# Kernel tuning notes

Measured on AMD Instinct MI355X. Metric: run time of the kernel, lower is better.

## Reference

```python
import jax, jax.numpy as jnp
import numpy as np

STRIDE = 4
IMG_H, IMG_W = 800, 1216
NMS_THRESH = 0.7
PRE_NMS = 1000
POST_NMS = 1000
MIN_SIZE = 0.0
SCALE_CLAMP = float(np.log(1000.0 / 16.0))  # detectron2 Box2BoxTransform clamp
A = 3  # anchors per location


def _cell_anchors():
    size = 32.0
    ars = jnp.array([0.5, 1.0, 2.0], jnp.float32)
    area = size * size
    w = jnp.sqrt(area / ars)
    h = ars * w
    return jnp.stack([-w / 2, -h / 2, w / 2, h / 2], axis=1)  # [A,4]


def _anchors(H, W):
    sx = jnp.arange(W, dtype=jnp.float32) * STRIDE
    sy = jnp.arange(H, dtype=jnp.float32) * STRIDE
    gy, gx = jnp.meshgrid(sy, sx, indexing='ij')
    shifts = jnp.stack([gx, gy, gx, gy], axis=-1).reshape(-1, 1, 4)  # [H*W,1,4]
    return (shifts + _cell_anchors()[None]).reshape(-1, 4)  # [H*W*A,4]


def _conv(x, w, b, pad):
    y = jax.lax.conv_general_dilated(x, w, (1, 1), pad,
                                     dimension_numbers=('NCHW', 'OIHW', 'NCHW'))
    return y + b[None, :, None, None]


def _decode(anchors, deltas):
    # anchors [M,4], deltas [N,M,4]; weights (1,1,1,1)
    wa = anchors[:, 2] - anchors[:, 0]
    ha = anchors[:, 3] - anchors[:, 1]
    cx = anchors[:, 0] + 0.5 * wa
    cy = anchors[:, 1] + 0.5 * ha
    dx, dy = deltas[..., 0], deltas[..., 1]
    dw = jnp.minimum(deltas[..., 2], SCALE_CLAMP)
    dh = jnp.minimum(deltas[..., 3], SCALE_CLAMP)
    px = dx * wa + cx
    py = dy * ha + cy
    pw = jnp.exp(dw) * wa
    ph = jnp.exp(dh) * ha
    return jnp.stack([px - 0.5 * pw, py - 0.5 * ph,
                      px + 0.5 * pw, py + 0.5 * ph], axis=-1)


def _iou_matrix(boxes):  # [K,4] -> [K,K]
    area = (boxes[:, 2] - boxes[:, 0]) * (boxes[:, 3] - boxes[:, 1])
    lt = jnp.maximum(boxes[:, None, :2], boxes[None, :, :2])
    rb = jnp.minimum(boxes[:, None, 2:], boxes[None, :, 2:])
    wh = jnp.clip(rb - lt, 0.0)
    inter = wh[..., 0] * wh[..., 1]
    return inter / jnp.maximum(area[:, None] + area[None, :] - inter, 1e-9)


def _nms_keep(boxes):
    # boxes already sorted by descending score; greedy NMS
    iou = _iou_matrix(boxes)
    K = boxes.shape[0]

    def step(sup, i):
        keep = ~sup[i]
        sup = sup | (keep & (iou[i] > NMS_THRESH))
        return sup, keep

    _, keep = jax.lax.scan(step, jnp.zeros(K, bool), jnp.arange(K))
    return keep


def setup_inputs() -> dict:
    key = jax.random.key(0)
    ks = jax.random.split(key, 4)
    features = jax.random.normal(ks[0], (2, 256, 200, 304), jnp.float32)
    w_conv = jax.random.normal(ks[1], (256, 256, 3, 3), jnp.float32) * 0.01
    b_conv = jnp.zeros((256,), jnp.float32)
    w_obj = jax.random.normal(ks[2], (3, 256, 1, 1), jnp.float32) * 0.01
    b_obj = jnp.zeros((3,), jnp.float32)
    w_delta = jax.random.normal(ks[3], (12, 256, 1, 1), jnp.float32) * 0.01
    b_delta = jnp.zeros((12,), jnp.float32)
    return {"features": features, "w_conv": w_conv, "b_conv": b_conv,
            "w_obj": w_obj, "b_obj": b_obj, "w_delta": w_delta, "b_delta": b_delta}


def reference(features, w_conv, b_conv, w_obj, b_obj, w_delta, b_delta):
    N, C, H, W = features.shape
    t = jax.nn.relu(_conv(features, w_conv, b_conv, 'SAME'))
    logits = _conv(t, w_obj, b_obj, 'VALID')            # [N,A,H,W]
    deltas = _conv(t, w_delta, b_delta, 'VALID')        # [N,4A,H,W]
    logits = logits.transpose(0, 2, 3, 1).reshape(N, -1)               # [N,H*W*A]
    deltas = deltas.reshape(N, A, 4, H, W).transpose(0, 3, 4, 1, 2).reshape(N, -1, 4)

    anchors = _anchors(H, W)                             # [H*W*A,4]
    boxes = _decode(anchors, deltas)                     # [N,M,4]
    boxes = jnp.stack([jnp.clip(boxes[..., 0], 0.0, IMG_W),
                       jnp.clip(boxes[..., 1], 0.0, IMG_H),
                       jnp.clip(boxes[..., 2], 0.0, IMG_W),
                       jnp.clip(boxes[..., 3], 0.0, IMG_H)], axis=-1)

    valid = ((boxes[..., 2] - boxes[..., 0]) >= MIN_SIZE) & \
            ((boxes[..., 3] - boxes[..., 1]) >= MIN_SIZE)
    scores = jnp.where(valid, logits, -jnp.inf)

    top_s, top_i = jax.lax.top_k(scores, PRE_NMS)                      # sorted desc
    top_b = jnp.take_along_axis(boxes, top_i[..., None], axis=1)       # [N,K,4]

    keep = jax.vmap(_nms_keep)(top_b)                                  # [N,K]
    s = jnp.where(keep, top_s, -jnp.inf)
    fin_s, fin_i = jax.lax.top_k(s, POST_NMS)                          # sorted desc (=final sort)
    fin_b = jnp.take_along_axis(top_b, fin_i[..., None], axis=1)
    fin_b = jnp.where(jnp.isfinite(fin_s)[..., None], fin_b, 0.0)
    return fin_b, fin_s
```

## Files before the change

kernel.cpp:

```cpp
#include <hip/hip_runtime.h>
#include <math.h>
#include <stdint.h>

#define CC 256
#define HH 200
#define WW 304
#define NN 2
#define HW 60800
#define MM 182400
#define KK 1000
#define HP 202
#define WP 306
#define SCALE_CLAMP_F 4.135166556742356f
#define NEG_SENTINEL -1.0e30f
#define CAND_CAP 2048

typedef __attribute__((ext_vector_type(8))) short short8;
typedef __attribute__((ext_vector_type(4))) float f32x4;

__device__ __forceinline__ unsigned short f2bf(float f) {
  unsigned u = __float_as_uint(f);
  u += 0x7FFFu + ((u >> 16) & 1u);
  return (unsigned short)(u >> 16);
}
__device__ __forceinline__ unsigned int fkey(float s) {
  unsigned int u = __float_as_uint(s);
  return (u & 0x80000000u) ? ~u : (u | 0x80000000u);
}
__device__ __forceinline__ float iou_ref(float4 a, float4 b) {
#pragma clang fp contract(off)
  float areaA = (a.z - a.x) * (a.w - a.y);
  float areaB = (b.z - b.x) * (b.w - b.y);
  float ltx = fmaxf(a.x, b.x), lty = fmaxf(a.y, b.y);
  float rbx = fminf(a.z, b.z), rby = fminf(a.w, b.w);
  float w = fmaxf(rbx - ltx, 0.0f), h = fmaxf(rby - lty, 0.0f);
  float inter = w * h;
  float denom = fmaxf(areaA + areaB - inter, 1e-9f);
  return inter / denom;
}
__device__ __forceinline__ void gload16(const void* g, void* l) {
  __builtin_amdgcn_global_load_lds(
      (const __attribute__((address_space(1))) unsigned int*)g,
      (__attribute__((address_space(3))) unsigned int*)l, 16, 0, 0);
}
__device__ __forceinline__ int swz(int byte) {
  return byte ^ (((byte >> 7) & 7) << 4);
}

__global__ __launch_bounds__(256) void pack_kernel(
    const float* __restrict__ w, unsigned short* __restrict__ wt_b,
    const float* __restrict__ in, unsigned short* __restrict__ fbp,
    unsigned int* __restrict__ ghist, unsigned int* __restrict__ cnt) {
  __shared__ unsigned short tile[64][65];
  int b = blockIdx.x;
  int tid = threadIdx.x;
  if (b < 2304) {
    int o = b * 256 + tid;
    int cin = o & 255, cout = (o >> 8) & 255, pos = o >> 16;
    wt_b[o] = f2bf(w[(cout * 256 + cin) * 9 + pos]);
  } else if (b < 10032) {
    int bb = b - 2304;
    int bx = bb % 966, rem = bb / 966;
    int by = rem & 3, n = rem >> 2;
    int p0 = bx * 64, c0 = by * 64;
    int lane = tid & 63;
    int p = p0 + lane;
    int yp = 0, xp = 0;
    bool inb = false;
    if (p < HP * WP) {
      yp = p / WP; xp = p - yp * WP;
      inb = (yp >= 1 && yp <= HH && xp >= 1 && xp <= WW);
    }
    for (int ci = tid >> 6; ci < 64; ci += 4) {
      float v = 0.f;
      if (inb) v = in[(((size_t)n * CC + c0 + ci) * HH + (yp - 1)) * WW + (xp - 1)];
      tile[ci][lane] = f2bf(v);
    }
    __syncthreads();
    for (int i = 0; i < 4; ++i) {
      int idx4 = (i * 256 + tid) * 4;
      int hwi = idx4 >> 6, cb = idx4 & 63;
      int pp = p0 + hwi;
      if (pp < HP * WP) {
        ushort4 v;
        v.x = tile[cb][hwi]; v.y = tile[cb + 1][hwi];
        v.z = tile[cb + 2][hwi]; v.w = tile[cb + 3][hwi];
        *(ushort4*)&fbp[((size_t)n * HP * WP + pp) * 256 + c0 + cb] = v;
      }
    }
  } else {
    int i = (b - 10032) * 256 + tid;
    ghist[i] = 0;
    if (i < 2) cnt[i] = 0;
  }
}

__global__ __launch_bounds__(256) void conv_mfma(
    const unsigned short* __restrict__ wt_b, const unsigned short* __restrict__ fbp,
    const float* __restrict__ bias, const float* __restrict__ w_obj,
    const float* __restrict__ w_delta, float* __restrict__ phead) {
  __shared__ __align__(16) unsigned short lA[2][4096];
  __shared__ __align__(16) unsigned short lB[2][5760];
  __shared__ float bl_l[128];
  int tid = threadIdx.x;
  int lane = tid & 63, wid = tid >> 6;
  int wm = wid >> 1, wn = wid & 1;
  int lrow = lane & 15, lgrp = lane >> 4;
  int zz = blockIdx.z;
  int n = zz >> 1, ct = zz & 1;
  int X0 = blockIdx.x * 16, Y0 = blockIdx.y * 8;

  f32x4 acc[4][4];
#pragma unroll
  for (int m = 0; m < 4; ++m)
#pragma unroll
    for (int r = 0; r < 4; ++r) acc[m][r] = {0.f, 0.f, 0.f, 0.f};

  if (tid < 128) bl_l[tid] = bias[ct * 128 + tid];

  auto stageA = [&](int pos, int cc, int buf) {
#pragma unroll
    for (int is = 0; is < 2; ++is) {
      int idx = is * 256 + tid;
      int L = swz(idx * 16);
      int cout = L >> 6, q = (L >> 4) & 3;
      const unsigned short* g =
          wt_b + (((size_t)pos * 256 + ct * 128 + cout) << 8) + cc * 32 + q * 8;
      gload16(g, (char*)&lA[buf][0] + is * 4096 + (wid << 10));
    }
  };
  auto stageB = [&](int cc, int buf) {
#pragma unroll
    for (int is = 0; is < 3; ++is) {
      int idx = is * 256 + tid;
      if (idx < 720) {
        int L = swz(idx * 16);
        int rc = L >> 6, q = (L >> 4) & 3;
        int row = rc / 18, col = rc - row * 18;
        const unsigned short* g =
            fbp + (((size_t)n * HP + Y0 + row) * WP + X0 + col) * 256 + cc * 32 + q * 8;
        gload16(g, (char*)&lB[buf][0] + is * 4096 + (wid << 10));
      }
    }
  };

  stageA(0, 0, 0);
  stageB(0, 0);
  __syncthreads();

  int ab = 0;
#pragma unroll 1
  for (int cc = 0; cc < 8; ++cc) {
    int bb = cc & 1;
#pragma unroll
    for (int pos = 0; pos < 9; ++pos) {
      if (pos < 8) stageA(pos + 1, cc, ab ^ 1);
      else if (cc < 7) stageA(0, cc + 1, ab ^ 1);
      if (pos == 0 && cc < 7) stageB(cc + 1, bb ^ 1);
      int ky = pos / 3, kx = pos - ky * 3;
      short8 af[4], bfr[4];
#pragma unroll
      for (int m = 0; m < 4; ++m) {
        int Lb = ((wm * 64 + m * 16 + lrow) << 6) + (lgrp << 4);
        af[m] = *(const short8*)((const char*)&lA[ab][0] + swz(Lb));
      }
#pragma unroll
      for (int r = 0; r < 4; ++r) {
        int Lb = (((wn * 4 + r + ky) * 18 + lrow + kx) << 6) + (lgrp << 4);
        bfr[r] = *(const short8*)((const char*)&lB[bb][0] + swz(Lb));
      }
#pragma unroll
      for (int m = 0; m < 4; ++m)
#pragma unroll
        for (int r = 0; r < 4; ++r)
          acc[m][r] = __builtin_amdgcn_mfma_f32_16x16x32_bf16(af[m], bfr[r], acc[m][r], 0, 0, 0);
      __syncthreads();
      ab ^= 1;
    }
  }

#pragma unroll
  for (int m = 0; m < 4; ++m)
#pragma unroll
    for (int j = 0; j < 4; ++j) {
      float b = bl_l[wm * 64 + m * 16 + (lgrp << 2) + j];
#pragma unroll
      for (int r = 0; r < 4; ++r) acc[m][r][j] = fmaxf(acc[m][r][j] + b, 0.f);
    }

  float* whl_l = (float*)&lA[0][0];
  for (int i = tid; i < 1920; i += 256) {
    int o = i >> 7, cl = i & 127;
    whl_l[i] = (o < 3) ? w_obj[o * 256 + ct * 128 + cl]
                       : w_delta[(o - 3) * 256 + ct * 128 + cl];
  }
  __syncthreads();

  float* hacc = (float*)&lB[0][0];
#pragma unroll 1
  for (int o = 0; o < 15; ++o) {
    float p0 = 0.f, p1 = 0.f, p2 = 0.f, p3 = 0.f;
#pragma unroll
    for (int m = 0; m < 4; ++m)
#pragma unroll
      for (int j = 0; j < 4; ++j) {
        float w = whl_l[o * 128 + wm * 64 + m * 16 + (lgrp << 2) + j];
        p0 = fmaf(w, acc[m][0][j], p0);
        p1 = fmaf(w, acc[m][1][j], p1);
        p2 = fmaf(w, acc[m][2][j], p2);
        p3 = fmaf(w, acc[m][3][j], p3);
      }
    p0 += __shfl_xor(p0, 16); p0 += __shfl_xor(p0, 32);
    p1 += __shfl_xor(p1, 16); p1 += __shfl_xor(p1, 32);
    p2 += __shfl_xor(p2, 16); p2 += __shfl_xor(p2, 32);
    p3 += __shfl_xor(p3, 16); p3 += __shfl_xor(p3, 32);
    if (lgrp == 0) {
      hacc[(((o * 8) + wn * 4 + 0) * 16 + lrow) * 2 + wm] = p0;
      hacc[(((o * 8) + wn * 4 + 1) * 16 + lrow) * 2 + wm] = p1;
      hacc[(((o * 8) + wn * 4 + 2) * 16 + lrow) * 2 + wm] = p2;
      hacc[(((o * 8) + wn * 4 + 3) * 16 + lrow) * 2 + wm] = p3;
    }
  }
  __syncthreads();

  if (tid < 128) {
    int row = tid >> 4, col = tid & 15;
    int loc = (Y0 + row) * WW + (X0 + col);
    size_t base = ((size_t)zz * 15) * HW + loc;
#pragma unroll
    for (int o = 0; o < 15; ++o) {
      const float* hp = &hacc[((o * 8 + row) * 16 + col) * 2];
      phead[base + (size_t)o * HW] = hp[0] + hp[1];
    }
  }
}

__global__ __launch_bounds__(256) void decode_kernel(
    const float* __restrict__ phead, const float* __restrict__ b_obj,
    const float* __restrict__ b_delta, float* __restrict__ scores,
    float* __restrict__ boxes, unsigned long long* __restrict__ keys,
    unsigned int* __restrict__ ghist) {
  __shared__ unsigned int hl[8192];
  int tid = threadIdx.x;
  for (int i = tid; i < 8192; i += 256) hl[i] = 0;
  __syncthreads();
  int n = blockIdx.y;
  int loc = blockIdx.x * 256 + tid;
  if (loc < HW) {
    float ho[15];
    const float* p0 = phead + ((size_t)(n * 2 + 0) * 15) * HW + loc;
    const float* p1 = phead + ((size_t)(n * 2 + 1) * 15) * HW + loc;
#pragma unroll
    for (int o = 0; o < 15; ++o) ho[o] = p0[(size_t)o * HW] + p1[(size_t)o * HW];
#pragma unroll
    for (int o = 0; o < 3; ++o) ho[o] += b_obj[o];
#pragma unroll
    for (int o = 0; o < 12; ++o) ho[3 + o] += b_delta[o];
    {
#pragma clang fp contract(off)
      int h = loc / WW, w = loc - h * WW;
      float gx = (float)(w * 4);
      float gy = (float)(h * 4);
      float s2048 = sqrtf(2048.0f), s512 = sqrtf(512.0f);
      float aw[3] = {s2048, 32.0f, s512};
      float ah[3] = {0.5f * s2048, 32.0f, 2.0f * s512};
#pragma unroll
      for (int a = 0; a < 3; ++a) {
        float ax1 = gx - 0.5f * aw[a], ay1 = gy - 0.5f * ah[a];
        float ax2 = gx + 0.5f * aw[a], ay2 = gy + 0.5f * ah[a];
        float wa = ax2 - ax1, ha = ay2 - ay1;
        float cx = ax1 + 0.5f * wa, cy = ay1 + 0.5f * ha;
        float dx = ho[3 + a * 4 + 0], dy = ho[3 + a * 4 + 1];
        float dw = fminf(ho[3 + a * 4 + 2], SCALE_CLAMP_F);
        float dh = fminf(ho[3 + a * 4 + 3], SCALE_CLAMP_F);
        float px = dx * wa + cx, py = dy * ha + cy;
        float pw = expf(dw) * wa, ph = expf(dh) * ha;
        float x1 = px - 0.5f * pw, y1 = py - 0.5f * ph;
        float x2v = px + 0.5f * pw, y2v = py + 0.5f * ph;
        x1 = fminf(fmaxf(x1, 0.f), 1216.f);
        y1 = fminf(fmaxf(y1, 0.f), 800.f);
        x2v = fminf(fmaxf(x2v, 0.f), 1216.f);
        y2v = fminf(fmaxf(y2v, 0.f), 800.f);
        int m = loc * 3 + a;
        ((float4*)boxes)[(size_t)n * MM + m] = make_float4(x1, y1, x2v, y2v);
        float sc = ho[a];
        scores[(size_t)n * MM + m] = sc;
        unsigned long long k =
            ((unsigned long long)fkey(sc) << 18) | (unsigned long long)(262143 - m);
        keys[(size_t)n * MM + m] = k;
        atomicAdd(&hl[(unsigned)(k >> 37)], 1u);
      }
    }
  }
  __syncthreads();
  for (int i = tid; i < 8192; i += 256) {
    unsigned v = hl[i];
    if (v) atomicAdd(&ghist[n * 8192 + i], v);
  }
}

__global__ __launch_bounds__(256) void gather_kernel(
    const unsigned long long* __restrict__ keys, const unsigned int* __restrict__ ghist,
    unsigned int* __restrict__ cnt, unsigned long long* __restrict__ cand) {
  __shared__ unsigned int ps[256];
  __shared__ int bsh;
  int n = blockIdx.y, tid = threadIdx.x;
  const unsigned int* h = ghist + n * 8192;
  unsigned s = 0;
  for (int k = 0; k < 32; ++k) s += h[tid * 32 + k];
  ps[tid] = s;
  __syncthreads();
  if (tid == 0) {
    unsigned cum = 0; int b = 0;
    for (int t = 255; t >= 0; --t) {
      if (cum + ps[t] >= KK) {
        for (int bin = t * 32 + 31; bin >= t * 32; --bin) {
          cum += h[bin];
          if (cum >= KK) { b = bin; break; }
        }
        break;
      }
      cum += ps[t];
    }
    bsh = b;
  }
  __syncthreads();
  int b = bsh;
  const unsigned long long* kp = keys + (size_t)n * MM;
  int i0 = blockIdx.x * 2850, i1 = min(i0 + 2850, MM);
  for (int i = i0 + tid; i < i1; i += 256) {
    unsigned long long k = kp[i];
    if ((int)(unsigned)(k >> 37) >= b) {
      unsigned pos = atomicAdd(&cnt[n], 1u);
      if (pos < CAND_CAP) cand[(size_t)n * CAND_CAP + pos] = k;
    }
  }
}

__global__ __launch_bounds__(1024) void final_select(
    const unsigned long long* __restrict__ cand, const unsigned int* __restrict__ cnt,
    const float* __restrict__ scores, const float* __restrict__ boxes,
    float* __restrict__ s_scores, float* __restrict__ s_boxes) {
  __shared__ unsigned long long sel[CAND_CAP];
  int n = blockIdx.x, tid = threadIdx.x;
  int E = (int)min(cnt[n], (unsigned)CAND_CAP);
  for (int i = tid; i < CAND_CAP; i += 1024)
    sel[i] = (i < E) ? cand[(size_t)n * CAND_CAP + i] : 0ull;
  __syncthreads();
  for (unsigned k2 = 2; k2 <= CAND_CAP; k2 <<= 1) {
    for (unsigned j = k2 >> 1; j > 0; j >>= 1) {
      for (int i = tid; i < CAND_CAP; i += 1024) {
        int l = i ^ (int)j;
        if (l > i) {
          unsigned long long a = sel[i], bb = sel[l];
          bool sw = ((i & k2) == 0) ? (a < bb) : (a > bb);
          if (sw) { sel[i] = bb; sel[l] = a; }
        }
      }
      __syncthreads();
    }
  }
  if (tid < KK) {
    unsigned long long k = sel[tid];
    int m = 262143 - (int)(k & 0x3FFFFull);
    s_scores[n * KK + tid] = scores[(size_t)n * MM + m];
    ((float4*)s_boxes)[n * KK + tid] = ((const float4*)boxes)[(size_t)n * MM + m];
  }
}

__global__ __launch_bounds__(256) void mask_kernel(const float* __restrict__ s_boxes,
                                                   unsigned long long* __restrict__ mask) {
  int i = blockIdx.x, n = blockIdx.y;
  int tid = threadIdx.x, w = tid >> 6, lane = tid & 63;
  const float4* bp = (const float4*)s_boxes + n * KK;
  float4 bi = bp[i];
#pragma unroll
  for (int p = 0; p < 4; ++p) {
    int word = p * 4 + w;
    int j = word * 64 + lane;
    bool over = false;
    if (j < KK) {
      float4 bj = bp[j];
      over = iou_ref(bi, bj) > 0.7f;
    }
    unsigned long long bal = __ballot(over);
    if (lane == 0) mask[((size_t)n * KK + i) * 16 + word] = bal;
  }
}

__global__ __launch_bounds__(1024) void scan_write_kernel(
    const float* __restrict__ s_scores, const float* __restrict__ s_boxes,
    const unsigned long long* __restrict__ mask, float* __restrict__ out) {
  int n = blockIdx.x, tid = threadIdx.x;
  int wid = tid >> 6, lane = tid & 63;
  __shared__ unsigned long long swl[16];
  __shared__ unsigned long long keepw[16];
  __shared__ unsigned int wpre[17];
  if (tid < 16) swl[tid] = 0ull;
  __syncthreads();
  const unsigned long long* mrow = mask + (size_t)n * 16000;
  for (int c = 0; c < 16; ++c) {
    int i = c * 64 + lane;
    unsigned long long myword = (i < KK) ? mrow[(size_t)i * 16 + wid] : 0ull;
    if (wid == 0) {
      unsigned long long m = (i < KK) ? mrow[(size_t)i * 16 + c] : 0ull;
      unsigned long long cur = swl[c];
      unsigned long long kw = 0ull;
      int lim = min(64, KK - c * 64);
      for (int b = 0; b < lim; ++b) {
        unsigned long long mb = __shfl(m, b);
        if (!((cur >> b) & 1ull)) { kw |= (1ull << b); cur |= mb; }
      }
      if (lane == 0) keepw[c] = kw;
    }
    __syncthreads();
    unsigned long long kw = keepw[c];
    unsigned long long v = ((kw >> lane) & 1ull) ? myword : 0ull;
#pragma unroll
    for (int s = 32; s > 0; s >>= 1) v |= __shfl_xor(v, s);
    if (lane == 0) swl[wid] |= v;
    __syncthreads();
  }
  if (tid == 0) {
    unsigned int c = 0;
    for (int w2 = 0; w2 < 16; ++w2) { wpre[w2] = c; c += (unsigned int)__popcll(keepw[w2]); }
    wpre[16] = c;
  }
  __syncthreads();
  if (tid < KK) {
    int word = tid >> 6, bit = tid & 63;
    unsigned long long kwv = keepw[word];
    bool kept = (kwv >> bit) & 1ull;
    unsigned int before = wpre[word] + (unsigned int)__popcll(kwv & ((1ull << bit) - 1ull));
    unsigned int nk = wpre[16];
    unsigned int dst = kept ? before : nk + ((unsigned int)tid - before);
    float4 b = kept ? ((const float4*)s_boxes)[n * KK + tid] : make_float4(0.f, 0.f, 0.f, 0.f);
    float s = kept ? s_scores[n * KK + tid] : NEG_SENTINEL;
    ((float4*)out)[n * KK + dst] = b;
    out[8000 + n * KK + dst] = s;
  }
}

extern "C" void kernel_launch(void* const* d_in, const int* in_sizes, int n_in,
                              void* d_out, int out_size, void* d_ws, size_t ws_size,
                              hipStream_t stream) {
  (void)in_sizes; (void)n_in; (void)out_size; (void)ws_size;
  const float* features = (const float*)d_in[0];
  const float* w_conv   = (const float*)d_in[1];
  const float* b_conv   = (const float*)d_in[2];
  const float* w_obj    = (const float*)d_in[3];
  const float* b_obj    = (const float*)d_in[4];
  const float* w_delta  = (const float*)d_in[5];
  const float* b_delta  = (const float*)d_in[6];

  char* ws = (char*)d_ws;
  unsigned short* wt_b = (unsigned short*)ws;
  unsigned short* fbp  = (unsigned short*)(ws + 1179648);
  char* O = ws + 64475136;
  float* phead = (float*)O;
  float* scores = (float*)(O + 14592000);
  float* boxes  = (float*)(O + 16051200);
  unsigned long long* keys = (unsigned long long*)(O + 21888000);
  char* P = O + 24806400;
  unsigned int* ghist = (unsigned int*)P;
  unsigned int* cnt = (unsigned int*)(P + 65536);
  unsigned long long* cand = (unsigned long long*)(P + 65792);
  float* s_scores = (float*)(P + 98560);
  float* s_boxes  = (float*)(P + 106752);
  unsigned long long* maskbuf = (unsigned long long*)(P + 139264);
  float* out = (float*)d_out;

  pack_kernel<<<10096, 256, 0, stream>>>(w_conv, wt_b, features, fbp, ghist, cnt);
  conv_mfma<<<dim3(19, 25, 4), 256, 0, stream>>>(wt_b, fbp, b_conv, w_obj, w_delta, phead);
  decode_kernel<<<dim3(238, 2), 256, 0, stream>>>(phead, b_obj, b_delta,
                                                  scores, boxes, keys, ghist);
  gather_kernel<<<dim3(64, 2), 256, 0, stream>>>(keys, ghist, cnt, cand);
  final_select<<<2, 1024, 0, stream>>>(cand, cnt, scores, boxes, s_scores, s_boxes);
  mask_kernel<<<dim3(1000, 2), 256, 0, stream>>>(s_boxes, maskbuf);
  scan_write_kernel<<<2, 1024, 0, stream>>>(s_scores, s_boxes, maskbuf, out);
}
```

Before: 388.5 us.

## Reuse conv B fragments across kx via DPP shifts; rank-select instead of bitonic sort

In the conv MFMA loop, B fragments for kx=0 and kx=2 are loaded once per ky row, and the kx=1 fragment is built from them with DPP lane shifts. This replaces one LDS read per tap with cross-lane moves, cutting LDS bandwidth for the B operand. Separately, final_select drops the 2048-element bitonic sort with its many barriers and computes each candidate's rank by counting larger keys, then scatters the top 1000 directly. Rank counting costs O(n^2) LDS reads per block but needs no synchronization rounds, and it relies on keys being unique.

Result: slower. 424.8 us (+9.3%).

```diff
diff --git a/kernel.cpp b/kernel.cpp
--- a/kernel.cpp
+++ b/kernel.cpp
@@ -45,6 +45,17 @@
 }
 __device__ __forceinline__ int swz(int byte) {
   return byte ^ (((byte >> 7) & 7) << 4);
+}
+__device__ __forceinline__ short8 mk_b1(short8 v0, short8 v2, bool hi15) {
+  union { short8 s; int i[4]; } a, c, o;
+  a.s = v0; c.s = v2;
+#pragma unroll
+  for (int w = 0; w < 4; ++w) {
+    int s = __builtin_amdgcn_mov_dpp(a.i[w], 0x111, 0xF, 0xF, true);
+    int t = __builtin_amdgcn_mov_dpp(c.i[w], 0x101, 0xF, 0xF, true);
+    o.i[w] = hi15 ? t : s;
+  }
+  return o.s;
 }
 
 __global__ __launch_bounds__(256) void pack_kernel(
@@ -106,6 +117,7 @@
   int lane = tid & 63, wid = tid >> 6;
   int wm = wid >> 1, wn = wid & 1;
   int lrow = lane & 15, lgrp = lane >> 4;
+  bool hi15 = (lrow == 15);
   int zz = blockIdx.z;
   int n = zz >> 1, ct = zz & 1;
   int X0 = blockIdx.x * 16, Y0 = blockIdx.y * 8;
@@ -153,29 +165,41 @@
   for (int cc = 0; cc < 8; ++cc) {
     int bb = cc & 1;
 #pragma unroll
-    for (int pos = 0; pos < 9; ++pos) {
-      if (pos < 8) stageA(pos + 1, cc, ab ^ 1);
-      else if (cc < 7) stageA(0, cc + 1, ab ^ 1);
-      if (pos == 0 && cc < 7) stageB(cc + 1, bb ^ 1);
-      int ky = pos / 3, kx = pos - ky * 3;
-      short8 af[4], bfr[4];
-#pragma unroll
-      for (int m = 0; m < 4; ++m) {
-        int Lb = ((wm * 64 + m * 16 + lrow) << 6) + (lgrp << 4);
-        af[m] = *(const short8*)((const char*)&lA[ab][0] + swz(Lb));
-      }
+    for (int ky = 0; ky < 3; ++ky) {
+      short8 b0[4], b2[4];
 #pragma unroll
       for (int r = 0; r < 4; ++r) {
-        int Lb = (((wn * 4 + r + ky) * 18 + lrow + kx) << 6) + (lgrp << 4);
-        bfr[r] = *(const short8*)((const char*)&lB[bb][0] + swz(Lb));
-      }
-#pragma unroll
-      for (int m = 0; m < 4; ++m)
+        int row = wn * 4 + r + ky;
+        int Lb0 = ((row * 18 + lrow) << 6) + (lgrp << 4);
+        int Lb2 = ((row * 18 + lrow + 2) << 6) + (lgrp << 4);
+        b0[r] = *(const short8*)((const char*)&lB[bb][0] + swz(Lb0));
+        b2[r] = *(const short8*)((const char*)&lB[bb][0] + swz(Lb2));
+      }
+#pragma unroll
+      for (int kx = 0; kx < 3; ++kx) {
+        int pos = ky * 3 + kx;
+        if (pos < 8) stageA(pos + 1, cc, ab ^ 1);
+        else if (cc < 7) stageA(0, cc + 1, ab ^ 1);
+        if (pos == 0 && cc < 7) stageB(cc + 1, bb ^ 1);
+        short8 af[4];
+#pragma unroll
+        for (int m = 0; m < 4; ++m) {
+          int Lb = ((wm * 64 + m * 16 + lrow) << 6) + (lgrp << 4);
+          af[m] = *(const short8*)((const char*)&lA[ab][0] + swz(Lb));
+        }
+        short8 bsel[4];
 #pragma unroll
         for (int r = 0; r < 4; ++r)
-          acc[m][r] = __builtin_amdgcn_mfma_f32_16x16x32_bf16(af[m], bfr[r], acc[m][r], 0, 0, 0);
-      __syncthreads();
-      ab ^= 1;
+          bsel[r] = (kx == 0) ? b0[r] : (kx == 2) ? b2[r] : mk_b1(b0[r], b2[r], hi15);
+#pragma unroll
+        for (int m = 0; m < 4; ++m)
+#pragma unroll
+          for (int r = 0; r < 4; ++r)
+            acc[m][r] =
+                __builtin_amdgcn_mfma_f32_16x16x32_bf16(af[m], bsel[r], acc[m][r], 0, 0, 0);
+        __syncthreads();
+        ab ^= 1;
+      }
     }
   }
 
@@ -347,24 +371,22 @@
   for (int i = tid; i < CAND_CAP; i += 1024)
     sel[i] = (i < E) ? cand[(size_t)n * CAND_CAP + i] : 0ull;
   __syncthreads();
-  for (unsigned k2 = 2; k2 <= CAND_CAP; k2 <<= 1) {
-    for (unsigned j = k2 >> 1; j > 0; j >>= 1) {
-      for (int i = tid; i < CAND_CAP; i += 1024) {
-        int l = i ^ (int)j;
-        if (l > i) {
-          unsigned long long a = sel[i], bb = sel[l];
-          bool sw = ((i & k2) == 0) ? (a < bb) : (a > bb);
-          if (sw) { sel[i] = bb; sel[l] = a; }
-        }
-      }
-      __syncthreads();
-    }
-  }
-  if (tid < KK) {
-    unsigned long long k = sel[tid];
-    int m = 262143 - (int)(k & 0x3FFFFull);
-    s_scores[n * KK + tid] = scores[(size_t)n * MM + m];
-    ((float4*)s_boxes)[n * KK + tid] = ((const float4*)boxes)[(size_t)n * MM + m];
+  unsigned long long k0 = sel[tid], k1 = sel[tid + 1024];
+  int r0 = 0, r1 = 0;
+  for (int j = 0; j < CAND_CAP; ++j) {
+    unsigned long long kj = sel[j];
+    r0 += (kj > k0);
+    r1 += (kj > k1);
+  }
+  if (r0 < KK && k0) {
+    int m = 262143 - (int)(k0 & 0x3FFFFull);
+    s_scores[n * KK + r0] = scores[(size_t)n * MM + m];
+    ((float4*)s_boxes)[n * KK + r0] = ((const float4*)boxes)[(size_t)n * MM + m];
+  }
+  if (r1 < KK && k1) {
+    int m = 262143 - (int)(k1 & 0x3FFFFull);
+    s_scores[n * KK + r1] = scores[(size_t)n * MM + m];
+    ((float4*)s_boxes)[n * KK + r1] = ((const float4*)boxes)[(size_t)n * MM + m];
   }
 }
 
```
